# Performance work log

Measured on AMD Instinct MI355X. Metric: run time of the kernel, lower is better.

## Reference

```python
import jax, jax.numpy as jnp
import numpy as np

N_NODES = 100000
N_EDGES = 1600000
IN_FEATS = 64
HIDDEN = 32
OUT_FEATS = 40


def _linear_init(key, fan_in, fan_out):
    kw, kb = jax.random.split(key)
    bound = 1.0 / np.sqrt(fan_in)
    W = jax.random.uniform(kw, (fan_in, fan_out), jnp.float32, -bound, bound)
    b = jax.random.uniform(kb, (fan_out,), jnp.float32, -bound, bound)
    return W, b


def setup_inputs() -> dict:
    key = jax.random.key(0)
    ks = jax.random.split(key, 8)
    x = jax.random.normal(ks[0], (N_NODES, IN_FEATS), jnp.float32)
    edge_index = jax.random.randint(ks[1], (2, N_EDGES), 0, N_NODES, jnp.int64)
    W_self1, b_self1 = _linear_init(ks[2], IN_FEATS, HIDDEN)
    W_neigh1, b_neigh1 = _linear_init(ks[3], IN_FEATS, HIDDEN)
    W_self2, b_self2 = _linear_init(ks[4], HIDDEN, HIDDEN)
    W_neigh2, b_neigh2 = _linear_init(ks[5], HIDDEN, HIDDEN)
    W_out, b_out = _linear_init(ks[6], HIDDEN, OUT_FEATS)
    W_lin1, b_lin1 = _linear_init(ks[7], IN_FEATS, OUT_FEATS)
    return {"x": x, "edge_index": edge_index,
            "W_self1": W_self1, "b_self1": b_self1,
            "W_neigh1": W_neigh1, "b_neigh1": b_neigh1,
            "W_self2": W_self2, "b_self2": b_self2,
            "W_neigh2": W_neigh2, "b_neigh2": b_neigh2,
            "W_out": W_out, "b_out": b_out,
            "W_lin1": W_lin1, "b_lin1": b_lin1}


def _scatter_mean(feats, src, dst, num_nodes):
    # gather neighbor features [E, F], sum into destinations, divide by degree
    msgs = feats[src]
    agg = jax.ops.segment_sum(msgs, dst, num_segments=num_nodes)
    cnt = jax.ops.segment_sum(jnp.ones((src.shape[0],), feats.dtype), dst,
                              num_segments=num_nodes)
    return agg / jnp.maximum(cnt, 1.0)[:, None]


def _intra_conv(h, src, dst, W_self, b_self, W_neigh, b_neigh, num_nodes):
    # scatter-mean aggregation + fused linear/residual(self)/relu
    x_self = h @ W_self + b_self
    neigh = _scatter_mean(h, src, dst, num_nodes)
    out = neigh @ W_neigh + b_neigh + x_self
    return jax.nn.relu(out)


def reference(x, edge_index, W_self1, b_self1, W_neigh1, b_neigh1,
              W_self2, b_self2, W_neigh2, b_neigh2, W_out, b_out,
              W_lin1, b_lin1):
    num_nodes = x.shape[0]
    src, dst = edge_index[0], edge_index[1]  # PyG source_to_target flow
    initial_x = x @ W_lin1 + b_lin1  # computed in original forward (unused in output)
    h = _intra_conv(x, src, dst, W_self1, b_self1, W_neigh1, b_neigh1, num_nodes)
    h = _intra_conv(h, src, dst, W_self2, b_self2, W_neigh2, b_neigh2, num_nodes)
    # hidden dim == 32 so x32 is the last layer's output (== h); dropout is eval no-op
    x32 = h
    logits = h @ W_out + b_out
    return (x32, logits)
```

## Files before the change

kernel.cpp:

```cpp
#include <hip/hip_runtime.h>

#define NN 100000
#define NE 1600000
#define RB 256
#define NPB 391
#define CAP 8192

typedef unsigned int uint;
typedef unsigned short ushort;
typedef __fp16 fp16x2 __attribute__((ext_vector_type(2)));

__device__ __forceinline__ float blo(uint u){ return __uint_as_float(u << 16); }
__device__ __forceinline__ float bhi(uint u){ return __uint_as_float(u & 0xffff0000u); }
__device__ __forceinline__ float b2f(ushort u){ return __uint_as_float(((uint)u) << 16); }
__device__ __forceinline__ ushort f2b(float f){
  uint u = __float_as_uint(f);
  uint r = (u + 0x7fffu + ((u >> 16) & 1u)) >> 16;
  return (ushort)r;
}
__device__ __forceinline__ uint packh2(float a, float b){
  union { fp16x2 h; uint u; } c; c.h = __builtin_amdgcn_cvt_pkrtz(a, b); return c.u;
}
__device__ __forceinline__ float h2lo(uint u){
  union { uint u; fp16x2 h; } c; c.u = u; return (float)c.h.x;
}
__device__ __forceinline__ float h2hi(uint u){
  union { uint u; fp16x2 h; } c; c.u = u; return (float)c.h.y;
}
__device__ __forceinline__ float ldf(const void* p, int i, bool isb){
  return isb ? b2f(((const ushort*)p)[i]) : ((const float*)p)[i];
}

__global__ void prep_k(const uint* __restrict__ xw,  const int* __restrict__ ei,
                       const void* __restrict__ Ws1, const void* __restrict__ bs1,
                       const void* __restrict__ Wn1, const void* __restrict__ bn1,
                       const void* __restrict__ Ws2, const void* __restrict__ bs2,
                       const void* __restrict__ Wn2, const void* __restrict__ bn2,
                       const void* __restrict__ Wo,  const void* __restrict__ bo,
                       float* __restrict__ wc1, float* __restrict__ bc1,
                       float* __restrict__ wc2, float* __restrict__ bc2,
                       float* __restrict__ wof, float* __restrict__ bof,
                       float* __restrict__ bn1f, float* __restrict__ bn2f,
                       int* __restrict__ flags, int* __restrict__ gcur)
{
  int t = threadIdx.x;
  __shared__ int nz, bcnt;
  __shared__ int s_isb;
  if (t == 0) { nz = 0; bcnt = 0; }
  __syncthreads();

  int hiw = ei[2 * t + 1];
  if (hiw != 0) atomicOr(&nz, 1);

  uint u = xw[t];
  uint le = (u >> 7) & 0xFFu;
  if (le == 0u || (le >= 96u && le <= 144u)) atomicAdd(&bcnt, 1);
  __syncthreads();
  if (t == 0) s_isb = (bcnt >= 240) ? 1 : 0;
  if (blockIdx.x == 0 && t == 0) {
    flags[0] = (bcnt >= 240) ? 1 : 0;
    flags[1] = (nz == 0) ? 1 : 0;
  }
  __syncthreads();
  bool isb = (s_isb != 0);

  if (blockIdx.x == 0) gcur[t] = t * CAP;

  int g0 = blockIdx.x * 256 + t, gs = gridDim.x * 256;
  for (int i = g0; i < 64 * 64; i += gs) {
    int f = i >> 6, j = i & 63;
    wc1[i] = (j < 32) ? ldf(Ws1, f * 32 + j, isb) : ldf(Wn1, f * 32 + (j - 32), isb);
  }
  for (int i = g0; i < 64; i += gs) bc1[i] = (i < 32) ? ldf(bs1, i, isb) : 0.f;
  for (int i = g0; i < 32 * 64; i += gs) {
    int f = i >> 6, j = i & 63;
    wc2[i] = (j < 32) ? ldf(Ws2, f * 32 + j, isb) : ldf(Wn2, f * 32 + (j - 32), isb);
  }
  for (int i = g0; i < 64; i += gs) bc2[i] = (i < 32) ? ldf(bs2, i, isb) : 0.f;
  for (int i = g0; i < 32 * 40; i += gs) wof[i] = ldf(Wo, i, isb);
  for (int i = g0; i < 40; i += gs) bof[i] = ldf(bo, i, isb);
  for (int i = g0; i < 32; i += gs) bn1f[i] = ldf(bn1, i, isb);
  for (int i = g0; i < 32; i += gs) bn2f[i] = ldf(bn2, i, isb);
}

__global__ __launch_bounds__(256) void part_k(const int* __restrict__ ei,
                                              const int* __restrict__ flags,
                                              int2* __restrict__ pairs,
                                              int* __restrict__ gcur, int E)
{
  __shared__ int hist[RB];
  __shared__ int gbase[RB];
  int m = flags[1];
  int base = blockIdx.x * 2048;
  hist[threadIdx.x] = 0;
  __syncthreads();
  int bk[8], rk[8]; int2 prs[8];
#pragma unroll
  for (int k = 0; k < 8; k++) {
    int e = base + threadIdx.x + k * 256;
    bk[k] = -1;
    if (e < E) {
      int d = m ? ei[2 * (E + e)] : ei[E + e];
      int s = m ? ei[2 * e] : ei[e];
      bk[k] = d / NPB;
      rk[k] = atomicAdd(&hist[bk[k]], 1);
      prs[k] = make_int2(d, s);
    }
  }
  __syncthreads();
  if (hist[threadIdx.x] > 0)
    gbase[threadIdx.x] = atomicAdd(&gcur[threadIdx.x], hist[threadIdx.x]);
  __syncthreads();
#pragma unroll
  for (int k = 0; k < 8; k++) {
    if (bk[k] >= 0) {
      int pos = gbase[bk[k]] + rk[k];
      if (pos < (bk[k] + 1) * CAP) pairs[pos] = prs[k];
    }
  }
}

__global__ __launch_bounds__(512) void csr_bucket_k(const int2* __restrict__ pairs,
                                                    const int* __restrict__ gcur,
                                                    int2* __restrict__ desc,
                                                    int* __restrict__ col)
{
  __shared__ int lh[NPB];
  __shared__ int ps[512];
  __shared__ int cs[RB];
  int t = threadIdx.x;
  int r = blockIdx.x;
  if (t < RB) cs[t] = min(gcur[t] - t * CAP, CAP);
  __syncthreads();
  if (t < RB) ps[t] = cs[t];
  __syncthreads();
  for (int off = 1; off < RB; off <<= 1) {
    int v = (t < RB && t >= off) ? ps[t - off] : 0;
    __syncthreads();
    if (t < RB) ps[t] += v;
    __syncthreads();
  }
  int n    = cs[r];
  int base = ps[r] - n;
  __syncthreads();

  int lo = r * NPB;
  int nn = min(NPB, NN - lo);
  int b0 = r * CAP;
  for (int j = t; j < NPB; j += 512) lh[j] = 0;
  __syncthreads();
  for (int i = b0 + t; i < b0 + n; i += 512)
    atomicAdd(&lh[pairs[i].x - lo], 1);
  __syncthreads();
  int v = (t < nn) ? lh[t] : 0;
  ps[t] = v;
  __syncthreads();
  for (int off = 1; off < 512; off <<= 1) {
    int x = (t >= off) ? ps[t - off] : 0;
    __syncthreads();
    ps[t] += x;
    __syncthreads();
  }
  int excl = base + ps[t] - v;
  if (t < nn) desc[lo + t] = make_int2(excl, v);
  __syncthreads();
  if (t < nn) lh[t] = excl;
  __syncthreads();
  for (int i = b0 + t; i < b0 + n; i += 512) {
    int2 pr = pairs[i];
    int p = atomicAdd(&lh[pr.x - lo], 1);
    col[p] = pr.y;
  }
}

template <int IN, bool XDYN>
__global__ __launch_bounds__(256) void transform_split_k(const void* __restrict__ xin,
                                                         const float* __restrict__ W,
                                                         const float* __restrict__ bias,
                                                         float* __restrict__ tself,
                                                         uint* __restrict__ tneigh,
                                                         const int* __restrict__ flags, int N)
{
  int n = blockIdx.x * 256 + threadIdx.x;
  if (n >= N) return;
  bool isb = XDYN ? (flags[0] != 0) : false;
  float xr[IN];
  if (XDYN && isb) {
    const uint4* p = (const uint4*)((const ushort*)xin + (size_t)n * IN);
#pragma unroll
    for (int k = 0; k < IN / 8; k++) {
      uint4 v = p[k];
      xr[8 * k + 0] = blo(v.x); xr[8 * k + 1] = bhi(v.x);
      xr[8 * k + 2] = blo(v.y); xr[8 * k + 3] = bhi(v.y);
      xr[8 * k + 4] = blo(v.z); xr[8 * k + 5] = bhi(v.z);
      xr[8 * k + 6] = blo(v.w); xr[8 * k + 7] = bhi(v.w);
    }
  } else {
    const float4* p = (const float4*)((const float*)xin + (size_t)n * IN);
#pragma unroll
    for (int k = 0; k < IN / 4; k++) {
      float4 v = p[k];
      xr[4 * k + 0] = v.x; xr[4 * k + 1] = v.y; xr[4 * k + 2] = v.z; xr[4 * k + 3] = v.w;
    }
  }
#pragma unroll 1
  for (int j0 = 0; j0 < 64; j0 += 32) {
    float acc[32];
#pragma unroll
    for (int jj = 0; jj < 32; jj++) acc[jj] = bias[j0 + jj];
#pragma unroll 8
    for (int f = 0; f < IN; f++) {
      float xv = xr[f];
#pragma unroll
      for (int jj = 0; jj < 32; jj++)
        acc[jj] = fmaf(xv, W[f * 64 + j0 + jj], acc[jj]);
    }
    if (j0 == 0) {
      float* o = tself + (size_t)n * 32;
#pragma unroll
      for (int q = 0; q < 8; q++)
        ((float4*)o)[q] = make_float4(acc[4 * q], acc[4 * q + 1], acc[4 * q + 2], acc[4 * q + 3]);
    } else {
      uint* o = tneigh + (size_t)n * 16;
#pragma unroll
      for (int q = 0; q < 4; q++) {
        uint4 v;
        v.x = packh2(acc[8 * q + 0], acc[8 * q + 1]);
        v.y = packh2(acc[8 * q + 2], acc[8 * q + 3]);
        v.z = packh2(acc[8 * q + 4], acc[8 * q + 5]);
        v.w = packh2(acc[8 * q + 6], acc[8 * q + 7]);
        ((uint4*)o)[q] = v;
      }
    }
  }
}

__global__ __launch_bounds__(256) void aggregate_k(const float* __restrict__ tself,
                                                   const uint* __restrict__ tneigh,
                                                   const int2* __restrict__ desc,
                                                   const int* __restrict__ col,
                                                   const float* __restrict__ bneigh,
                                                   float* __restrict__ hout,
                                                   void* __restrict__ out2,
                                                   const float* __restrict__ Wo,
                                                   const float* __restrict__ bo,
                                                   const int* __restrict__ flags, int N)
{
  __shared__ float hsh[4][32];
  int w = threadIdx.x >> 6;
  int d = blockIdx.x * 4 + w;
  int lane = threadIdx.x & 63;
  int slot = lane >> 3, f4 = lane & 7;
  int2 dd = desc[d];
  int start = dd.x, deg = dd.y, end = start + deg;
  float a0 = 0.f, a1 = 0.f, a2 = 0.f, a3 = 0.f;
  for (int base = start; base < end; base += 64) {
    int cnt = min(64, end - base);
    int ce = (lane < cnt) ? col[base + lane] : 0;
#pragma unroll 1
    for (int j = 0; j < cnt; j += 16) {
      int k0 = j + slot, k1 = j + 8 + slot;
      int i0 = __shfl(ce, k0, 64);
      int i1 = __shfl(ce, k1, 64);
      uint2 u0 = make_uint2(0, 0), u1 = make_uint2(0, 0);
      if (k0 < cnt) u0 = ((const uint2*)(tneigh + (size_t)i0 * 16))[f4];
      if (k1 < cnt) u1 = ((const uint2*)(tneigh + (size_t)i1 * 16))[f4];
      a0 += h2lo(u0.x) + h2lo(u1.x);
      a1 += h2hi(u0.x) + h2hi(u1.x);
      a2 += h2lo(u0.y) + h2lo(u1.y);
      a3 += h2hi(u0.y) + h2hi(u1.y);
    }
  }
  a0 += __shfl_down(a0, 8, 64);  a1 += __shfl_down(a1, 8, 64);
  a2 += __shfl_down(a2, 8, 64);  a3 += __shfl_down(a3, 8, 64);
  a0 += __shfl_down(a0, 16, 64); a1 += __shfl_down(a1, 16, 64);
  a2 += __shfl_down(a2, 16, 64); a3 += __shfl_down(a3, 16, 64);
  a0 += __shfl_down(a0, 32, 64); a1 += __shfl_down(a1, 32, 64);
  a2 += __shfl_down(a2, 32, 64); a3 += __shfl_down(a3, 32, 64);
  bool isb = (flags[0] != 0);
  if (lane < 8) {
    float scale = 1.0f / (float)max(deg, 1);
    float4 self = ((const float4*)(tself + (size_t)d * 32))[lane];
    float4 bn   = ((const float4*)bneigh)[lane];
    float v0 = fmaxf(fmaf(a0, scale, bn.x + self.x), 0.f);
    float v1 = fmaxf(fmaf(a1, scale, bn.y + self.y), 0.f);
    float v2 = fmaxf(fmaf(a2, scale, bn.z + self.z), 0.f);
    float v3 = fmaxf(fmaf(a3, scale, bn.w + self.w), 0.f);
    if (hout) ((float4*)(hout + (size_t)d * 32))[lane] = make_float4(v0, v1, v2, v3);
    if (out2) {
      if (isb) {
        uint2 pk;
        pk.x = (uint)f2b(v0) | ((uint)f2b(v1) << 16);
        pk.y = (uint)f2b(v2) | ((uint)f2b(v3) << 16);
        ((uint2*)out2)[(size_t)d * 8 + lane] = pk;
      } else {
        ((float4*)out2)[(size_t)d * 8 + lane] = make_float4(v0, v1, v2, v3);
      }
    }
    hsh[w][4 * lane] = v0; hsh[w][4 * lane + 1] = v1;
    hsh[w][4 * lane + 2] = v2; hsh[w][4 * lane + 3] = v3;
  }
  if (Wo) {
    __syncthreads();
    if (lane < 40) {
      float acc = bo[lane];
#pragma unroll 8
      for (int f = 0; f < 32; f++)
        acc = fmaf(hsh[w][f], Wo[f * 40 + lane], acc);
      size_t idx = (size_t)N * 32 + (size_t)d * 40 + lane;
      if (isb) ((ushort*)out2)[idx] = f2b(acc);
      else     ((float*)out2)[idx] = acc;
    }
  }
}

extern "C" void kernel_launch(void* const* d_in, const int* in_sizes, int n_in,
                              void* d_out, int out_size, void* d_ws, size_t ws_size,
                              hipStream_t stream)
{
  const int N = NN, E = NE;
  const void* x   = d_in[0];
  const int*  ei  = (const int*)d_in[1];

  char* p = (char*)d_ws;
  auto alloc = [&](size_t bytes) -> void* {
    void* r = (void*)p;
    p += (bytes + 255) & ~(size_t)255;
    return r;
  };
  float* wc1  = (float*)alloc(64 * 64 * 4);
  float* bc1  = (float*)alloc(64 * 4);
  float* wc2  = (float*)alloc(32 * 64 * 4);
  float* bc2  = (float*)alloc(64 * 4);
  float* wof  = (float*)alloc(32 * 40 * 4);
  float* bof  = (float*)alloc(40 * 4);
  float* bn1f = (float*)alloc(32 * 4);
  float* bn2f = (float*)alloc(32 * 4);
  int*   flags = (int*)alloc(8);
  int*   gcur = (int*)alloc(RB * 4);
  int2*  desc = (int2*)alloc((size_t)N * 8);
  int*   col  = (int*)alloc((size_t)E * 4);
  int2*  pairs = (int2*)alloc((size_t)RB * CAP * 8);
  float* tself  = (float*)alloc((size_t)N * 32 * 4);
  uint*  tneigh = (uint*)alloc((size_t)N * 16 * 4);
  float* hbuf = (float*)alloc((size_t)N * 32 * 4);

  prep_k<<<17, 256, 0, stream>>>((const uint*)x, ei,
                                 d_in[2], d_in[3], d_in[4], d_in[5],
                                 d_in[6], d_in[7], d_in[8], d_in[9],
                                 d_in[10], d_in[11],
                                 wc1, bc1, wc2, bc2, wof, bof, bn1f, bn2f,
                                 flags, gcur);
  part_k<<<(E + 2047) / 2048, 256, 0, stream>>>(ei, flags, pairs, gcur, E);
  csr_bucket_k<<<RB, 512, 0, stream>>>(pairs, gcur, desc, col);

  transform_split_k<64, true><<<(N + 255) / 256, 256, 0, stream>>>(
      x, wc1, bc1, tself, tneigh, flags, N);
  aggregate_k<<<N / 4, 256, 0, stream>>>(tself, tneigh, desc, col, bn1f,
                                         hbuf, (void*)nullptr,
                                         (const float*)nullptr, (const float*)nullptr,
                                         flags, N);

  transform_split_k<32, false><<<(N + 255) / 256, 256, 0, stream>>>(
      hbuf, wc2, bc2, tself, tneigh, flags, N);
  aggregate_k<<<N / 4, 256, 0, stream>>>(tself, tneigh, desc, col, bn2f,
                                         (float*)nullptr, d_out,
                                         wof, bof, flags, N);
}
```

Before: 287.4 us.

## Fuse partition with layer-1 transform and layer-2 transform into aggregation

Merges the edge partition kernel and the first-layer node transform into one launch via block-index dispatch, so the two independent stages can overlap. Folds the second-layer transform into the first aggregation using wave shuffles, which drops the intermediate hidden buffer write and read and one launch. The output aggregation now computes logits through shuffles instead of shared memory plus a barrier. It reuses the pairs buffer for tneigh2 and adds shuffle-heavy per-wave matmuls that every lane executes.

After: 273.0 us. 5.0% less time.

```diff
diff --git a/kernel.cpp b/kernel.cpp
--- a/kernel.cpp
+++ b/kernel.cpp
@@ -83,15 +83,15 @@
   for (int i = g0; i < 32; i += gs) bn2f[i] = ldf(bn2, i, isb);
 }
 
-__global__ __launch_bounds__(256) void part_k(const int* __restrict__ ei,
-                                              const int* __restrict__ flags,
-                                              int2* __restrict__ pairs,
-                                              int* __restrict__ gcur, int E)
+__device__ __forceinline__ void part_body(const int* __restrict__ ei,
+                                          const int* __restrict__ flags,
+                                          int2* __restrict__ pairs,
+                                          int* __restrict__ gcur, int E, int blk)
 {
   __shared__ int hist[RB];
   __shared__ int gbase[RB];
   int m = flags[1];
-  int base = blockIdx.x * 2048;
+  int base = blk * 2048;
   hist[threadIdx.x] = 0;
   __syncthreads();
   int bk[8], rk[8]; int2 prs[8];
@@ -100,11 +100,11 @@
     int e = base + threadIdx.x + k * 256;
     bk[k] = -1;
     if (e < E) {
-      int d = m ? ei[2 * (E + e)] : ei[E + e];
-      int s = m ? ei[2 * e] : ei[e];
-      bk[k] = d / NPB;
+      int dd = m ? ei[2 * (E + e)] : ei[E + e];
+      int s  = m ? ei[2 * e] : ei[e];
+      bk[k] = dd / NPB;
       rk[k] = atomicAdd(&hist[bk[k]], 1);
-      prs[k] = make_int2(d, s);
+      prs[k] = make_int2(dd, s);
     }
   }
   __syncthreads();
@@ -120,69 +120,14 @@
   }
 }
 
-__global__ __launch_bounds__(512) void csr_bucket_k(const int2* __restrict__ pairs,
-                                                    const int* __restrict__ gcur,
-                                                    int2* __restrict__ desc,
-                                                    int* __restrict__ col)
-{
-  __shared__ int lh[NPB];
-  __shared__ int ps[512];
-  __shared__ int cs[RB];
-  int t = threadIdx.x;
-  int r = blockIdx.x;
-  if (t < RB) cs[t] = min(gcur[t] - t * CAP, CAP);
-  __syncthreads();
-  if (t < RB) ps[t] = cs[t];
-  __syncthreads();
-  for (int off = 1; off < RB; off <<= 1) {
-    int v = (t < RB && t >= off) ? ps[t - off] : 0;
-    __syncthreads();
-    if (t < RB) ps[t] += v;
-    __syncthreads();
-  }
-  int n    = cs[r];
-  int base = ps[r] - n;
-  __syncthreads();
-
-  int lo = r * NPB;
-  int nn = min(NPB, NN - lo);
-  int b0 = r * CAP;
-  for (int j = t; j < NPB; j += 512) lh[j] = 0;
-  __syncthreads();
-  for (int i = b0 + t; i < b0 + n; i += 512)
-    atomicAdd(&lh[pairs[i].x - lo], 1);
-  __syncthreads();
-  int v = (t < nn) ? lh[t] : 0;
-  ps[t] = v;
-  __syncthreads();
-  for (int off = 1; off < 512; off <<= 1) {
-    int x = (t >= off) ? ps[t - off] : 0;
-    __syncthreads();
-    ps[t] += x;
-    __syncthreads();
-  }
-  int excl = base + ps[t] - v;
-  if (t < nn) desc[lo + t] = make_int2(excl, v);
-  __syncthreads();
-  if (t < nn) lh[t] = excl;
-  __syncthreads();
-  for (int i = b0 + t; i < b0 + n; i += 512) {
-    int2 pr = pairs[i];
-    int p = atomicAdd(&lh[pr.x - lo], 1);
-    col[p] = pr.y;
-  }
-}
-
 template <int IN, bool XDYN>
-__global__ __launch_bounds__(256) void transform_split_k(const void* __restrict__ xin,
-                                                         const float* __restrict__ W,
-                                                         const float* __restrict__ bias,
-                                                         float* __restrict__ tself,
-                                                         uint* __restrict__ tneigh,
-                                                         const int* __restrict__ flags, int N)
-{
-  int n = blockIdx.x * 256 + threadIdx.x;
-  if (n >= N) return;
+__device__ __forceinline__ void transform_body(const void* __restrict__ xin,
+                                               const float* __restrict__ W,
+                                               const float* __restrict__ bias,
+                                               float* __restrict__ tself,
+                                               uint* __restrict__ tneigh,
+                                               const int* __restrict__ flags, int n)
+{
   bool isb = XDYN ? (flags[0] != 0) : false;
   float xr[IN];
   if (XDYN && isb) {
@@ -235,21 +180,86 @@
   }
 }
 
-__global__ __launch_bounds__(256) void aggregate_k(const float* __restrict__ tself,
-                                                   const uint* __restrict__ tneigh,
-                                                   const int2* __restrict__ desc,
-                                                   const int* __restrict__ col,
-                                                   const float* __restrict__ bneigh,
-                                                   float* __restrict__ hout,
-                                                   void* __restrict__ out2,
-                                                   const float* __restrict__ Wo,
-                                                   const float* __restrict__ bo,
-                                                   const int* __restrict__ flags, int N)
-{
-  __shared__ float hsh[4][32];
-  int w = threadIdx.x >> 6;
-  int d = blockIdx.x * 4 + w;
-  int lane = threadIdx.x & 63;
+__global__ __launch_bounds__(256) void part_t1_k(const int* __restrict__ ei,
+                                                 const int* __restrict__ flags,
+                                                 int2* __restrict__ pairs,
+                                                 int* __restrict__ gcur, int E,
+                                                 const void* __restrict__ x,
+                                                 const float* __restrict__ wc1,
+                                                 const float* __restrict__ bc1,
+                                                 float* __restrict__ tself,
+                                                 uint* __restrict__ tneigh,
+                                                 int N, int PB)
+{
+  if ((int)blockIdx.x < PB) {
+    part_body(ei, flags, pairs, gcur, E, (int)blockIdx.x);
+  } else {
+    int n = ((int)blockIdx.x - PB) * 256 + threadIdx.x;
+    if (n < N) transform_body<64, true>(x, wc1, bc1, tself, tneigh, flags, n);
+  }
+}
+
+__global__ __launch_bounds__(512) void csr_bucket_k(const int2* __restrict__ pairs,
+                                                    const int* __restrict__ gcur,
+                                                    int2* __restrict__ desc,
+                                                    int* __restrict__ col)
+{
+  __shared__ int lh[NPB];
+  __shared__ int ps[512];
+  __shared__ int cs[RB];
+  int t = threadIdx.x;
+  int r = blockIdx.x;
+  if (t < RB) cs[t] = min(gcur[t] - t * CAP, CAP);
+  __syncthreads();
+  if (t < RB) ps[t] = cs[t];
+  __syncthreads();
+  for (int off = 1; off < RB; off <<= 1) {
+    int v = (t < RB && t >= off) ? ps[t - off] : 0;
+    __syncthreads();
+    if (t < RB) ps[t] += v;
+    __syncthreads();
+  }
+  int n    = cs[r];
+  int base = ps[r] - n;
+  __syncthreads();
+
+  int lo = r * NPB;
+  int nn = min(NPB, NN - lo);
+  int b0 = r * CAP;
+  for (int j = t; j < NPB; j += 512) lh[j] = 0;
+  __syncthreads();
+  for (int i = b0 + t; i < b0 + n; i += 512)
+    atomicAdd(&lh[pairs[i].x - lo], 1);
+  __syncthreads();
+  int v = (t < nn) ? lh[t] : 0;
+  ps[t] = v;
+  __syncthreads();
+  for (int off = 1; off < 512; off <<= 1) {
+    int x = (t >= off) ? ps[t - off] : 0;
+    __syncthreads();
+    ps[t] += x;
+    __syncthreads();
+  }
+  int excl = base + ps[t] - v;
+  if (t < nn) desc[lo + t] = make_int2(excl, v);
+  __syncthreads();
+  if (t < nn) lh[t] = excl;
+  __syncthreads();
+  for (int i = b0 + t; i < b0 + n; i += 512) {
+    int2 pr = pairs[i];
+    int p = atomicAdd(&lh[pr.x - lo], 1);
+    col[p] = pr.y;
+  }
+}
+
+__device__ __forceinline__ void agg_core(const float* __restrict__ tself,
+                                         const uint* __restrict__ tneigh,
+                                         const int2* __restrict__ desc,
+                                         const int* __restrict__ col,
+                                         const float* __restrict__ bneigh,
+                                         int d, int lane,
+                                         float& v0, float& v1, float& v2, float& v3)
+{
   int slot = lane >> 3, f4 = lane & 7;
   int2 dd = desc[d];
   int start = dd.x, deg = dd.y, end = start + deg;
@@ -271,46 +281,99 @@
       a3 += h2hi(u0.y) + h2hi(u1.y);
     }
   }
-  a0 += __shfl_down(a0, 8, 64);  a1 += __shfl_down(a1, 8, 64);
-  a2 += __shfl_down(a2, 8, 64);  a3 += __shfl_down(a3, 8, 64);
-  a0 += __shfl_down(a0, 16, 64); a1 += __shfl_down(a1, 16, 64);
-  a2 += __shfl_down(a2, 16, 64); a3 += __shfl_down(a3, 16, 64);
-  a0 += __shfl_down(a0, 32, 64); a1 += __shfl_down(a1, 32, 64);
-  a2 += __shfl_down(a2, 32, 64); a3 += __shfl_down(a3, 32, 64);
+  a0 += __shfl_xor(a0, 8, 64);  a1 += __shfl_xor(a1, 8, 64);
+  a2 += __shfl_xor(a2, 8, 64);  a3 += __shfl_xor(a3, 8, 64);
+  a0 += __shfl_xor(a0, 16, 64); a1 += __shfl_xor(a1, 16, 64);
+  a2 += __shfl_xor(a2, 16, 64); a3 += __shfl_xor(a3, 16, 64);
+  a0 += __shfl_xor(a0, 32, 64); a1 += __shfl_xor(a1, 32, 64);
+  a2 += __shfl_xor(a2, 32, 64); a3 += __shfl_xor(a3, 32, 64);
+  float scale = 1.0f / (float)max(deg, 1);
+  float4 self = ((const float4*)(tself + (size_t)d * 32))[f4];
+  float4 bn   = ((const float4*)bneigh)[f4];
+  v0 = fmaxf(fmaf(a0, scale, bn.x + self.x), 0.f);
+  v1 = fmaxf(fmaf(a1, scale, bn.y + self.y), 0.f);
+  v2 = fmaxf(fmaf(a2, scale, bn.z + self.z), 0.f);
+  v3 = fmaxf(fmaf(a3, scale, bn.w + self.w), 0.f);
+}
+
+__device__ __forceinline__ float hfeat(int f, float v0, float v1, float v2, float v3)
+{
+  int src = f >> 2;
+  switch (f & 3) {
+    case 0:  return __shfl(v0, src, 64);
+    case 1:  return __shfl(v1, src, 64);
+    case 2:  return __shfl(v2, src, 64);
+    default: return __shfl(v3, src, 64);
+  }
+}
+
+__global__ __launch_bounds__(256) void agg_t2_k(const float* __restrict__ tself1,
+                                                const uint* __restrict__ tneigh1,
+                                                const int2* __restrict__ desc,
+                                                const int* __restrict__ col,
+                                                const float* __restrict__ bn1f,
+                                                const float* __restrict__ wc2,
+                                                const float* __restrict__ bc2,
+                                                float* __restrict__ tself2,
+                                                uint* __restrict__ tneigh2)
+{
+  int w = threadIdx.x >> 6;
+  int d = blockIdx.x * 4 + w;
+  int lane = threadIdx.x & 63;
+  float v0, v1, v2, v3;
+  agg_core(tself1, tneigh1, desc, col, bn1f, d, lane, v0, v1, v2, v3);
+  float acc = bc2[lane];
+#pragma unroll
+  for (int f = 0; f < 32; f++)
+    acc = fmaf(hfeat(f, v0, v1, v2, v3), wc2[f * 64 + lane], acc);
+  if (lane < 32)
+    tself2[(size_t)d * 32 + lane] = acc;
+  float pl = __shfl(acc, 32 + 2 * (lane & 15), 64);
+  float ph = __shfl(acc, 33 + 2 * (lane & 15), 64);
+  if (lane < 16)
+    tneigh2[(size_t)d * 16 + lane] = packh2(pl, ph);
+}
+
+__global__ __launch_bounds__(256) void agg_out_k(const float* __restrict__ tself2,
+                                                 const uint* __restrict__ tneigh2,
+                                                 const int2* __restrict__ desc,
+                                                 const int* __restrict__ col,
+                                                 const float* __restrict__ bn2f,
+                                                 const float* __restrict__ wof,
+                                                 const float* __restrict__ bof,
+                                                 void* __restrict__ out,
+                                                 const int* __restrict__ flags)
+{
+  int w = threadIdx.x >> 6;
+  int d = blockIdx.x * 4 + w;
+  int lane = threadIdx.x & 63;
+  float v0, v1, v2, v3;
+  agg_core(tself2, tneigh2, desc, col, bn2f, d, lane, v0, v1, v2, v3);
   bool isb = (flags[0] != 0);
   if (lane < 8) {
-    float scale = 1.0f / (float)max(deg, 1);
-    float4 self = ((const float4*)(tself + (size_t)d * 32))[lane];
-    float4 bn   = ((const float4*)bneigh)[lane];
-    float v0 = fmaxf(fmaf(a0, scale, bn.x + self.x), 0.f);
-    float v1 = fmaxf(fmaf(a1, scale, bn.y + self.y), 0.f);
-    float v2 = fmaxf(fmaf(a2, scale, bn.z + self.z), 0.f);
-    float v3 = fmaxf(fmaf(a3, scale, bn.w + self.w), 0.f);
-    if (hout) ((float4*)(hout + (size_t)d * 32))[lane] = make_float4(v0, v1, v2, v3);
-    if (out2) {
-      if (isb) {
-        uint2 pk;
-        pk.x = (uint)f2b(v0) | ((uint)f2b(v1) << 16);
-        pk.y = (uint)f2b(v2) | ((uint)f2b(v3) << 16);
-        ((uint2*)out2)[(size_t)d * 8 + lane] = pk;
-      } else {
-        ((float4*)out2)[(size_t)d * 8 + lane] = make_float4(v0, v1, v2, v3);
-      }
-    }
-    hsh[w][4 * lane] = v0; hsh[w][4 * lane + 1] = v1;
-    hsh[w][4 * lane + 2] = v2; hsh[w][4 * lane + 3] = v3;
-  }
-  if (Wo) {
-    __syncthreads();
-    if (lane < 40) {
-      float acc = bo[lane];
-#pragma unroll 8
-      for (int f = 0; f < 32; f++)
-        acc = fmaf(hsh[w][f], Wo[f * 40 + lane], acc);
-      size_t idx = (size_t)N * 32 + (size_t)d * 40 + lane;
-      if (isb) ((ushort*)out2)[idx] = f2b(acc);
-      else     ((float*)out2)[idx] = acc;
-    }
+    if (isb) {
+      uint2 pk;
+      pk.x = (uint)f2b(v0) | ((uint)f2b(v1) << 16);
+      pk.y = (uint)f2b(v2) | ((uint)f2b(v3) << 16);
+      ((uint2*)out)[(size_t)d * 8 + lane] = pk;
+    } else {
+      ((float4*)out)[(size_t)d * 8 + lane] = make_float4(v0, v1, v2, v3);
+    }
+  }
+  int lj = (lane < 40) ? lane : 39;
+  float acc = bof[lj];
+#pragma unroll
+  for (int f = 0; f < 32; f++)
+    acc = fmaf(hfeat(f, v0, v1, v2, v3), wof[f * 40 + lj], acc);
+  if (isb) {
+    float lo = __shfl(acc, 2 * lane, 64);
+    float hi = __shfl(acc, 2 * lane + 1, 64);
+    if (lane < 20)
+      ((uint*)out)[(size_t)NN * 16 + (size_t)d * 20 + lane] =
+          (uint)f2b(lo) | ((uint)f2b(hi) << 16);
+  } else {
+    if (lane < 40)
+      ((float*)out)[(size_t)NN * 32 + (size_t)d * 40 + lane] = acc;
   }
 }
 
@@ -341,9 +404,13 @@
   int2*  desc = (int2*)alloc((size_t)N * 8);
   int*   col  = (int*)alloc((size_t)E * 4);
   int2*  pairs = (int2*)alloc((size_t)RB * CAP * 8);
-  float* tself  = (float*)alloc((size_t)N * 32 * 4);
-  uint*  tneigh = (uint*)alloc((size_t)N * 16 * 4);
-  float* hbuf = (float*)alloc((size_t)N * 32 * 4);
+  float* tself1 = (float*)alloc((size_t)N * 32 * 4);
+  uint*  tneigh1 = (uint*)alloc((size_t)N * 16 * 4);
+  float* tself2 = (float*)alloc((size_t)N * 32 * 4);
+  uint*  tneigh2 = (uint*)pairs;
+
+  const int PB = (E + 2047) / 2048;
+  const int TB = (N + 255) / 256;
 
   prep_k<<<17, 256, 0, stream>>>((const uint*)x, ei,
                                  d_in[2], d_in[3], d_in[4], d_in[5],
@@ -351,19 +418,11 @@
                                  d_in[10], d_in[11],
                                  wc1, bc1, wc2, bc2, wof, bof, bn1f, bn2f,
                                  flags, gcur);
-  part_k<<<(E + 2047) / 2048, 256, 0, stream>>>(ei, flags, pairs, gcur, E);
+  part_t1_k<<<PB + TB, 256, 0, stream>>>(ei, flags, pairs, gcur, E,
+                                         x, wc1, bc1, tself1, tneigh1, N, PB);
   csr_bucket_k<<<RB, 512, 0, stream>>>(pairs, gcur, desc, col);
-
-  transform_split_k<64, true><<<(N + 255) / 256, 256, 0, stream>>>(
-      x, wc1, bc1, tself, tneigh, flags, N);
-  aggregate_k<<<N / 4, 256, 0, stream>>>(tself, tneigh, desc, col, bn1f,
-                                         hbuf, (void*)nullptr,
-                                         (const float*)nullptr, (const float*)nullptr,
-                                         flags, N);
-
-  transform_split_k<32, false><<<(N + 255) / 256, 256, 0, stream>>>(
-      hbuf, wc2, bc2, tself, tneigh, flags, N);
-  aggregate_k<<<N / 4, 256, 0, stream>>>(tself, tneigh, desc, col, bn2f,
-                                         (float*)nullptr, d_out,
-                                         wof, bof, flags, N);
-}
+  agg_t2_k<<<N / 4, 256, 0, stream>>>(tself1, tneigh1, desc, col, bn1f,
+                                      wc2, bc2, tself2, tneigh2);
+  agg_out_k<<<N / 4, 256, 0, stream>>>(tself2, tneigh2, desc, col, bn2f,
+                                       wof, bof, d_out, flags);
+}
```
